# Performance work log

Measured on AMD Instinct MI355X. Metric: run time of the kernel, lower is better.

The kernel has to match this reference:

```python
import jax, jax.numpy as jnp
import numpy as np

NUM_HEADS = 32
NUM_KV_HEADS = 8
HEAD_DIM = 128
NEG_INF = -1e9


def rotate_half(x):
    x1, x2 = jnp.split(x, 2, axis=-1)
    return jnp.concatenate([-x2, x1], axis=-1)


def setup_inputs() -> dict:
    key = jax.random.key(0)
    ks = jax.random.split(key, 8)
    B, S, H = 2, 2048, 4096
    hidden_states = jax.random.normal(ks[0], (B, S, H), jnp.float32) * 0.02
    # additive causal mask [1,1,S,S]: 0 on/below diagonal, -1e9 above
    causal = jnp.tril(jnp.ones((S, S), bool))
    attention_mask = jnp.where(causal, 0.0, NEG_INF)[None, None, :, :].astype(jnp.float32)
    # RoPE tables (theta=500000 style), shape [1,S,head_dim]
    inv_freq = 1.0 / (500000.0 ** (np.arange(0, HEAD_DIM, 2, dtype=np.float32) / HEAD_DIM))
    t = np.arange(S, dtype=np.float32)
    freqs = np.outer(t, inv_freq)  # [S, head_dim/2]
    emb = np.concatenate([freqs, freqs], axis=-1)  # [S, head_dim]
    cos = jnp.asarray(np.cos(emb))[None]
    sin = jnp.asarray(np.sin(emb))[None]
    scale = 0.02
    wq = jax.random.normal(ks[1], (NUM_HEADS * HEAD_DIM, H), jnp.float32) * scale
    wk = jax.random.normal(ks[2], (NUM_KV_HEADS * HEAD_DIM, H), jnp.float32) * scale
    wv = jax.random.normal(ks[3], (NUM_KV_HEADS * HEAD_DIM, H), jnp.float32) * scale
    wo = jax.random.normal(ks[4], (H, NUM_HEADS * HEAD_DIM), jnp.float32) * scale
    return {"hidden_states": hidden_states, "attention_mask": attention_mask,
            "cos": cos, "sin": sin, "wq": wq, "wk": wk, "wv": wv, "wo": wo}


def reference(hidden_states, attention_mask, cos, sin, wq, wk, wv, wo):
    B, S, H = hidden_states.shape
    nh, nkv, hd = NUM_HEADS, NUM_KV_HEADS, HEAD_DIM
    groups = nh // nkv
    # QKV projections (bias=False)
    q = jnp.einsum('bsh,dh->bsd', hidden_states, wq).reshape(B, S, nh, hd).transpose(0, 2, 1, 3)
    k = jnp.einsum('bsh,dh->bsd', hidden_states, wk).reshape(B, S, nkv, hd).transpose(0, 2, 1, 3)
    v = jnp.einsum('bsh,dh->bsd', hidden_states, wv).reshape(B, S, nkv, hd).transpose(0, 2, 1, 3)
    # RoPE: cos/sin [1,S,hd] -> broadcast over head dim [1,1,S,hd]
    c = cos[:, None, :, :]
    s = sin[:, None, :, :]
    q = q * c + rotate_half(q) * s
    k = k * c + rotate_half(k) * s
    # GQA: repeat_kv
    k = jnp.repeat(k, groups, axis=1)  # [B,nh,S,hd]
    v = jnp.repeat(v, groups, axis=1)
    # SDPA with additive mask
    scores = jnp.einsum('bhqd,bhkd->bhqk', q, k) / jnp.sqrt(jnp.float32(hd))
    scores = scores + attention_mask[:, :, :, :k.shape[2]]
    attn = jax.nn.softmax(scores, axis=-1)
    out = jnp.einsum('bhqk,bhkd->bhqd', attn, v)  # [B,nh,S,hd]
    out = out.transpose(0, 2, 1, 3).reshape(B, S, nh * hd)
    return jnp.einsum('bsd,hd->bsh', out, wo)
```

## Files before the change

kernel.cpp:

```cpp
#include <hip/hip_runtime.h>
#include <hip/hip_bf16.h>

typedef __attribute__((ext_vector_type(8))) __bf16 bf16x8;
typedef __attribute__((ext_vector_type(4))) float f32x4;
typedef __attribute__((ext_vector_type(16))) float f32x16;
typedef __attribute__((ext_vector_type(4))) unsigned int u32x4;

#define SEQ 2048
#define NH 32
#define NKV 8
#define HD 128

__device__ __forceinline__ ushort f2bf(float f) {
  unsigned u = __builtin_bit_cast(unsigned, f);
  unsigned r = (u + 0x7fffu + ((u >> 16) & 1u)) >> 16;
  return (ushort)r;
}
__device__ __forceinline__ float bf2f(ushort h) {
  return __builtin_bit_cast(float, ((unsigned)h) << 16);
}
__device__ __forceinline__ unsigned cvt_pk_bf16(float lo, float hi) {
  unsigned r;
  asm("v_cvt_pk_bf16_f32 %0, %1, %2" : "=v"(r) : "v"(lo), "v"(hi));
  return r;
}
__device__ __forceinline__ float exp2_fast(float x) {
  float r;
  asm("v_exp_f32 %0, %1" : "=v"(r) : "v"(x));
  return r;
}
__device__ __forceinline__ void gload16(const void* g, void* l) {
  __builtin_amdgcn_global_load_lds(
      (const __attribute__((address_space(1))) void*)g,
      (__attribute__((address_space(3))) void*)l, 16, 0, 0);
}

__global__ __launch_bounds__(256) void f2bf5_kernel(const float4* __restrict__ hs,
                                                    const float4* __restrict__ wq,
                                                    const float4* __restrict__ wk,
                                                    const float4* __restrict__ wv,
                                                    const float4* __restrict__ wo,
                                                    ushort4* __restrict__ out) {
  unsigned i = blockIdx.x * 256 + threadIdx.x;
  const float4* src;
  unsigned j;
  if (i < 4194304u) { src = hs; j = i; }
  else if (i < 8388608u) { src = wq; j = i - 4194304u; }
  else if (i < 9437184u) { src = wk; j = i - 8388608u; }
  else if (i < 10485760u) { src = wv; j = i - 9437184u; }
  else { src = wo; j = i - 10485760u; }
  float4 v = src[j];
  ushort4 o;
  o.x = f2bf(v.x); o.y = f2bf(v.y); o.z = f2bf(v.z); o.w = f2bf(v.w);
  out[i] = o;
}

template <int OUTF32>
__global__ __launch_bounds__(256) void gemm_bt_kernel(const ushort* __restrict__ A,
                                                      const ushort* __restrict__ B,
                                                      void* __restrict__ C,
                                                      int M, int N, int K) {
  __shared__ ushort As[2][128 * 32];
  __shared__ ushort Bs[2][128 * 32];
  const int tid = threadIdx.x;
  const int w = tid >> 6, l = tid & 63;
  const int lr = l & 15, lc = l >> 4;
  const int bx = blockIdx.x, by = blockIdx.y;
  const int wr = w >> 1, wc = w & 1;

  f32x4 z = {0.f, 0.f, 0.f, 0.f};
  f32x4 acc[4][4];
#pragma unroll
  for (int i = 0; i < 4; ++i)
#pragma unroll
    for (int j = 0; j < 4; ++j) acc[i][j] = z;

  const ushort* aSrc = A + (size_t)(by * 128 + 32 * w + (l >> 2)) * K + (l & 3) * 8;
  const ushort* bSrc = B + (size_t)(bx * 128 + 32 * w + (l >> 2)) * K + (l & 3) * 8;
  const int ldsOff = (32 * w) * 32;

#pragma unroll
  for (int q = 0; q < 2; ++q) {
    gload16(aSrc + (size_t)q * 16 * K, &As[0][ldsOff + q * 512]);
    gload16(bSrc + (size_t)q * 16 * K, &Bs[0][ldsOff + q * 512]);
  }
  __syncthreads();

  const int nk = K >> 5;
  int cur = 0;
  for (int kt = 0; kt < nk; ++kt) {
    if (kt + 1 < nk) {
      const ushort* a2 = aSrc + (size_t)(kt + 1) * 32;
      const ushort* b2 = bSrc + (size_t)(kt + 1) * 32;
#pragma unroll
      for (int q = 0; q < 2; ++q) {
        gload16(a2 + (size_t)q * 16 * K, &As[cur ^ 1][ldsOff + q * 512]);
        gload16(b2 + (size_t)q * 16 * K, &Bs[cur ^ 1][ldsOff + q * 512]);
      }
    }
    bf16x8 af[4], bfr[4];
#pragma unroll
    for (int i = 0; i < 4; ++i)
      af[i] = *(const bf16x8*)&As[cur][(64 * wr + 16 * i + lr) * 32 + lc * 8];
#pragma unroll
    for (int j = 0; j < 4; ++j)
      bfr[j] = *(const bf16x8*)&Bs[cur][(64 * wc + 16 * j + lr) * 32 + lc * 8];
#pragma unroll
    for (int i = 0; i < 4; ++i)
#pragma unroll
      for (int j = 0; j < 4; ++j)
        acc[i][j] = __builtin_amdgcn_mfma_f32_16x16x32_bf16(af[i], bfr[j], acc[i][j], 0, 0, 0);
    __syncthreads();
    cur ^= 1;
  }

#pragma unroll
  for (int i = 0; i < 4; ++i)
#pragma unroll
    for (int j = 0; j < 4; ++j) {
      int row = by * 128 + 64 * wr + 16 * i + lc * 4;
      int col = bx * 128 + 64 * wc + 16 * j + lr;
#pragma unroll
      for (int r = 0; r < 4; ++r) {
        if (OUTF32)
          ((float*)C)[(size_t)(row + r) * N + col] = acc[i][j][r];
        else
          ((ushort*)C)[(size_t)(row + r) * N + col] = f2bf(acc[i][j][r]);
      }
    }
}

template <int OUTF32>
__global__ __launch_bounds__(512, 2) void gemm256_kernel(const ushort* __restrict__ A,
                                                         const ushort* __restrict__ B,
                                                         void* __restrict__ C,
                                                         int M, int N, int K) {
  __shared__ ushort As[2][256 * 64];
  __shared__ ushort Bs[2][256 * 64];
  const int tid = threadIdx.x;
  const int w = tid >> 6, l = tid & 63;
  const int lr = l & 15, lc = l >> 4;
  const int wr = w >> 2, wc = w & 3;

  const int nbx = N >> 8;
  const int cpx = gridDim.x >> 3;
  const int sw = (blockIdx.x & 7) * cpx + (blockIdx.x >> 3);
  const int bx = sw % nbx, by = sw / nbx;

  const ushort* Asrc = A + (size_t)(by * 256) * K;
  const ushort* Bsrc = B + (size_t)(bx * 256) * K;

  f32x4 z = {0.f, 0.f, 0.f, 0.f};
  f32x4 acc[8][4];
#pragma unroll
  for (int m = 0; m < 8; ++m)
#pragma unroll
    for (int n = 0; n < 4; ++n) acc[m][n] = z;

  const int NK = K >> 6;

  auto stage = [&](int kt2, int s) {
    if (kt2 >= NK) return;
    const int mat = s >> 1, half = s & 1;
    const ushort* g = mat ? Bsrc : Asrc;
    char* lb = (char*)(mat ? &Bs[kt2 & 1][0] : &As[kt2 & 1][0]) + half * 16384 + w * 1024;
#pragma unroll
    for (int i = 0; i < 2; ++i) {
      int row = half * 128 + i * 64 + w * 8 + (l >> 3);
      int csw = ((l & 7) * 16) ^ ((row & 7) << 4);
      gload16(g + (size_t)row * K + kt2 * 64 + (csw >> 1), lb + i * 8192);
    }
  };

  stage(0, 0); stage(0, 1); stage(0, 2); stage(0, 3);
  stage(1, 0);

  bf16x8 af[4][2], bfr[4][2];
  for (int kt = 0; kt < NK; ++kt) {
    const char* Ab = (const char*)&As[kt & 1][0];
    const char* Bb = (const char*)&Bs[kt & 1][0];
    if (kt + 1 < NK) asm volatile("s_waitcnt vmcnt(2)" ::: "memory");
    else             asm volatile("s_waitcnt vmcnt(0)" ::: "memory");
    asm volatile("s_barrier" ::: "memory");

#pragma unroll
    for (int m = 0; m < 4; ++m) {
      int row = wr * 128 + m * 16 + lr;
#pragma unroll
      for (int ks = 0; ks < 2; ++ks)
        af[m][ks] = *(const bf16x8*)(Ab + row * 128 + ((ks * 64 + lc * 16) ^ ((row & 7) << 4)));
    }
#pragma unroll
    for (int n = 0; n < 2; ++n) {
      int row = wc * 64 + n * 16 + lr;
#pragma unroll
      for (int ks = 0; ks < 2; ++ks)
        bfr[n][ks] = *(const bf16x8*)(Bb + row * 128 + ((ks * 64 + lc * 16) ^ ((row & 7) << 4)));
    }
    stage(kt + 1, 1);
    __builtin_amdgcn_s_setprio(1);
#pragma unroll
    for (int m = 0; m < 4; ++m)
#pragma unroll
      for (int n = 0; n < 2; ++n)
#pragma unroll
        for (int ks = 0; ks < 2; ++ks)
          acc[m][n] = __builtin_amdgcn_mfma_f32_16x16x32_bf16(af[m][ks], bfr[n][ks], acc[m][n], 0, 0, 0);
    __builtin_amdgcn_s_setprio(0);
    asm volatile("s_barrier" ::: "memory");

#pragma unroll
    for (int n = 2; n < 4; ++n) {
      int row = wc * 64 + n * 16 + lr;
#pragma unroll
      for (int ks = 0; ks < 2; ++ks)
        bfr[n][ks] = *(const bf16x8*)(Bb + row * 128 + ((ks * 64 + lc * 16) ^ ((row & 7) << 4)));
    }
    stage(kt + 1, 2);
    __builtin_amdgcn_s_setprio(1);
#pragma unroll
    for (int m = 0; m < 4; ++m)
#pragma unroll
      for (int n = 2; n < 4; ++n)
#pragma unroll
        for (int ks = 0; ks < 2; ++ks)
          acc[m][n] = __builtin_amdgcn_mfma_f32_16x16x32_bf16(af[m][ks], bfr[n][ks], acc[m][n], 0, 0, 0);
    __builtin_amdgcn_s_setprio(0);
    asm volatile("s_barrier" ::: "memory");

#pragma unroll
    for (int m = 0; m < 4; ++m) {
      int row = wr * 128 + (m + 4) * 16 + lr;
#pragma unroll
      for (int ks = 0; ks < 2; ++ks)
        af[m][ks] = *(const bf16x8*)(Ab + row * 128 + ((ks * 64 + lc * 16) ^ ((row & 7) << 4)));
    }
    stage(kt + 1, 3);
    __builtin_amdgcn_s_setprio(1);
#pragma unroll
    for (int m = 0; m < 4; ++m)
#pragma unroll
      for (int n = 0; n < 2; ++n)
#pragma unroll
        for (int ks = 0; ks < 2; ++ks)
          acc[m + 4][n] = __builtin_amdgcn_mfma_f32_16x16x32_bf16(af[m][ks], bfr[n][ks], acc[m + 4][n], 0, 0, 0);
    __builtin_amdgcn_s_setprio(0);
    asm volatile("s_barrier" ::: "memory");

    stage(kt + 2, 0);
    __builtin_amdgcn_s_setprio(1);
#pragma unroll
    for (int m = 0; m < 4; ++m)
#pragma unroll
      for (int n = 2; n < 4; ++n)
#pragma unroll
        for (int ks = 0; ks < 2; ++ks)
          acc[m + 4][n] = __builtin_amdgcn_mfma_f32_16x16x32_bf16(af[m][ks], bfr[n][ks], acc[m + 4][n], 0, 0, 0);
    __builtin_amdgcn_s_setprio(0);
  }

#pragma unroll
  for (int m = 0; m < 8; ++m)
#pragma unroll
    for (int n = 0; n < 4; ++n) {
      int row = by * 256 + wr * 128 + m * 16 + lc * 4;
      int col = bx * 256 + wc * 64 + n * 16 + lr;
#pragma unroll
      for (int r = 0; r < 4; ++r) {
        if (OUTF32)
          ((float*)C)[(size_t)(row + r) * N + col] = acc[m][n][r];
        else
          ((ushort*)C)[(size_t)(row + r) * N + col] = f2bf(acc[m][n][r]);
      }
    }
}

__global__ __launch_bounds__(256) void relayout_kernel(const ushort* __restrict__ q_lin,
                                                       const ushort* __restrict__ kv_lin,
                                                       const float* __restrict__ cosb,
                                                       const float* __restrict__ sinb,
                                                       ushort* __restrict__ Qh,
                                                       ushort* __restrict__ Kh,
                                                       ushort* __restrict__ Vt,
                                                       float qscale) {
  __shared__ ushort t[64][66];
  const unsigned bid = blockIdx.x;
  if (bid < 40960u) {
    const bool isQ = bid < 32768u;
    const ushort* in = isQ ? q_lin : kv_lin;
    ushort* out = isQ ? Qh : Kh;
    const int ld = isQ ? 4096 : 2048;
    const int hshift = isQ ? 5 : 3;
    const float scale = isQ ? qscale : 1.0f;
    int idx = (isQ ? bid : (bid - 32768u)) * 256 + threadIdx.x;
    int d = idx & 63;
    int nh = 1 << hshift;
    int h = (idx >> 6) & (nh - 1);
    int rowg = idx >> (6 + hshift);
    int s = rowg & (SEQ - 1);
    int b = rowg >> 11;
    const ushort* p = in + (size_t)rowg * ld + h * HD + d;
    float x = bf2f(p[0]), y = bf2f(p[64]);
    float c = cosb[s * HD + d], sn = sinb[s * HD + d];
    ushort* qo = out + (((size_t)(b * nh + h)) * SEQ + s) * HD + d;
    qo[0] = f2bf((x * c - y * sn) * scale);
    qo[64] = f2bf((y * c + x * sn) * scale);
  } else {
    unsigned i = bid - 40960u;
    const int s0 = (i & 31) * 64;
    const int c0 = ((i >> 5) & 15) * 64;
    const int b = i >> 9;
    const int tx = threadIdx.x & 63;
    const int ty = threadIdx.x >> 6;
#pragma unroll
    for (int rr = 0; rr < 64; rr += 4) {
      int r = rr + ty;
      t[r][tx] = kv_lin[((size_t)(b * SEQ + s0 + r)) * 2048 + 1024 + c0 + tx];
    }
    __syncthreads();
#pragma unroll
    for (int rr = 0; rr < 64; rr += 4) {
      int c = rr + ty;
      int cg = c0 + c;
      int kvh = cg >> 7, d = cg & 127;
      Vt[(((size_t)(b * NKV + kvh)) * HD + d) * SEQ + s0 + tx] = t[tx][c];
    }
  }
}

__global__ __launch_bounds__(512, 2) void attn_kernel(const ushort* __restrict__ Qh,
                                                      const ushort* __restrict__ Kh,
                                                      const ushort* __restrict__ Vt,
                                                      ushort* __restrict__ Out) {
  __shared__ ushort Kl[2][64 * 128];
  __shared__ ushort Vl[2][128 * 64];

  const int tid = threadIdx.x;
  const int w = tid >> 6, l = tid & 63;
  const int lq = l & 31;
  const int hl = l >> 5;
  const int g = w >> 2;
  const int wl = w & 3;

  const int n = blockIdx.x;
  const int xcd = n & 7, i = n >> 3;
  const int qpi = i & 7;
  const int h2 = (i >> 3) & 3;
  const int pp = 2 * xcd + (i >> 5);
  const int bb = pp >> 3, kvh = pp & 7;
  const int hh = kvh * 4 + h2;
  const int bh = bb * 32 + hh;
  const int qt = g ? (15 - qpi) : qpi;
  const int q0 = qt * 128;
  const int wrow0 = q0 + 32 * wl;
  const int qrow = wrow0 + lq;

  const ushort* Kbase = Kh + ((size_t)(bb * NKV + kvh) * SEQ) * HD;
  const ushort* Vbase = Vt + ((size_t)(bb * NKV + kvh) * HD) * SEQ;

  bf16x8 qf[8];
  {
    const ushort* qrp = Qh + ((size_t)bh * SEQ + qrow) * HD + 8 * hl;
#pragma unroll
    for (int s8 = 0; s8 < 8; ++s8) qf[s8] = *(const bf16x8*)(qrp + 16 * s8);
  }

  f32x16 o[4];
#pragma unroll
  for (int db = 0; db < 4; ++db)
#pragma unroll
    for (int i2 = 0; i2 < 16; ++i2) o[db][i2] = 0.f;
  float m_run = -1e30f, l_run = 0.f;

  const int ntw = 2 * qt + (wl >> 1) + 1;
  const int ntb = 2 * (15 - qpi) + 2;

  auto stageKV = [&](int buf, int t) {
    const int kv0 = t * 64;
#pragma unroll
    for (int q = 0; q < 2; ++q) {
      int c = 2 * w + q;
      int row = c * 4 + (l >> 4);
      int cs = ((l & 15) ^ (row & 7)) * 8;
      gload16(Kbase + ((size_t)(kv0 + row)) * HD + cs, &Kl[buf][c * 512]);
    }
#pragma unroll
    for (int q = 0; q < 2; ++q) {
      int c = 2 * w + q;
      int row = c * 8 + (l >> 3);
      int cs = ((l & 7) ^ (row & 7)) * 8;
      gload16(Vbase + (size_t)row * SEQ + kv0 + cs, &Vl[buf][c * 512]);
    }
  };

  stageKV(0, 0);
  __syncthreads();

  int cur = 0;
  for (int t = 0; t < ntb; ++t) {
    const int kv0 = t * 64;
    if (t + 1 < ntb) stageKV(cur ^ 1, t + 1);

    if (t < ntw) {
      f32x16 sacc[2];
#pragma unroll
      for (int b2 = 0; b2 < 2; ++b2)
#pragma unroll
        for (int i2 = 0; i2 < 16; ++i2) sacc[b2][i2] = 0.f;

      const int swz = lq & 7;
      __builtin_amdgcn_s_setprio(1);
#pragma unroll
      for (int s8 = 0; s8 < 8; ++s8) {
#pragma unroll
        for (int b2 = 0; b2 < 2; ++b2) {
          int row = 32 * b2 + lq;
          bf16x8 kf = *(const bf16x8*)((const char*)&Kl[cur][0] + row * 256 +
                                       (((2 * s8 + hl) ^ swz) << 4));
          sacc[b2] = __builtin_amdgcn_mfma_f32_32x32x16_bf16(kf, qf[s8], sacc[b2], 0, 0, 0);
        }
      }
      __builtin_amdgcn_s_setprio(0);

      if (t == ntw - 1) {
#pragma unroll
        for (int b2 = 0; b2 < 2; ++b2)
#pragma unroll
          for (int r2 = 0; r2 < 16; ++r2) {
            int kv = kv0 + 32 * b2 + (r2 & 3) + 8 * (r2 >> 2) + 4 * hl;
            if (kv > qrow) sacc[b2][r2] = -1e30f;
          }
      }

      float tm[8];
#pragma unroll
      for (int r2 = 0; r2 < 8; ++r2)
        tm[r2] = fmaxf(fmaxf(sacc[0][r2], sacc[0][r2 + 8]),
                       fmaxf(sacc[1][r2], sacc[1][r2 + 8]));
#pragma unroll
      for (int s2 = 4; s2; s2 >>= 1)
#pragma unroll
        for (int r2 = 0; r2 < s2; ++r2) tm[r2] = fmaxf(tm[r2], tm[r2 + s2]);
      float mx = fmaxf(tm[0], __shfl_xor(tm[0], 32));

      if (__any(mx > m_run + 8.0f)) {
        float mn = fmaxf(m_run, mx);
        float sc = exp2_fast(m_run - mn);
        m_run = mn;
        l_run *= sc;
#pragma unroll
        for (int db = 0; db < 4; ++db) o[db] *= sc;
      }

#pragma unroll
      for (int b2 = 0; b2 < 2; ++b2)
#pragma unroll
        for (int r2 = 0; r2 < 16; ++r2) sacc[b2][r2] = exp2_fast(sacc[b2][r2] - m_run);
      float ts[8];
#pragma unroll
      for (int r2 = 0; r2 < 8; ++r2)
        ts[r2] = (sacc[0][r2] + sacc[0][r2 + 8]) + (sacc[1][r2] + sacc[1][r2 + 8]);
#pragma unroll
      for (int s2 = 4; s2; s2 >>= 1)
#pragma unroll
        for (int r2 = 0; r2 < s2; ++r2) ts[r2] += ts[r2 + s2];
      l_run += ts[0] + __shfl_xor(ts[0], 32);

      unsigned pw[2][8];
#pragma unroll
      for (int b2 = 0; b2 < 2; ++b2)
#pragma unroll
        for (int i2 = 0; i2 < 8; ++i2)
          pw[b2][i2] = cvt_pk_bf16(sacc[b2][2 * i2], sacc[b2][2 * i2 + 1]);

#pragma unroll
      for (int s = 0; s < 4; ++s) {
        const int b2 = s >> 1, bs = 4 * (s & 1);
        unsigned wA = pw[b2][bs], wB = pw[b2][bs + 1], wC = pw[b2][bs + 2], wD = pw[b2][bs + 3];
        unsigned s1 = hl ? wA : wC, s2v = hl ? wB : wD;
        unsigned rx1 = (unsigned)__shfl_xor((int)s1, 32);
        unsigned rx2 = (unsigned)__shfl_xor((int)s2v, 32);
        u32x4 fw = {hl ? rx1 : wA, hl ? rx2 : wB, hl ? wC : rx1, hl ? wD : rx2};
        bf16x8 pfrag = __builtin_bit_cast(bf16x8, fw);
        bf16x8 vf[4];
#pragma unroll
        for (int db = 0; db < 4; ++db) {
          int row = 32 * db + lq;
          vf[db] = *(const bf16x8*)((const char*)&Vl[cur][0] + row * 128 +
                                    (((2 * s + hl) ^ swz) << 4));
        }
        __builtin_amdgcn_s_setprio(1);
#pragma unroll
        for (int db = 0; db < 4; ++db)
          o[db] = __builtin_amdgcn_mfma_f32_32x32x16_bf16(vf[db], pfrag, o[db], 0, 0, 0);
        __builtin_amdgcn_s_setprio(0);
      }
    }
    __syncthreads();
    cur ^= 1;
  }

  const float inv = 1.0f / l_run;
  ushort* outp = Out + ((size_t)bb * SEQ + qrow) * (NH * HD) + hh * HD;
#pragma unroll
  for (int db = 0; db < 4; ++db)
#pragma unroll
    for (int i2 = 0; i2 < 8; ++i2) {
      unsigned wrd = cvt_pk_bf16(o[db][2 * i2] * inv, o[db][2 * i2 + 1] * inv);
      int d = 32 * db + 2 * (i2 & 1) + 8 * (i2 >> 1) + 4 * hl;
      *(unsigned*)(outp + d) = wrd;
    }
}

extern "C" void kernel_launch(void* const* d_in, const int* in_sizes, int n_in,
                              void* d_out, int out_size, void* d_ws, size_t ws_size,
                              hipStream_t stream) {
  const float* hs = (const float*)d_in[0];
  const float* cosb = (const float*)d_in[2];
  const float* sinb = (const float*)d_in[3];
  const float* wq = (const float*)d_in[4];
  const float* wk = (const float*)d_in[5];
  const float* wv = (const float*)d_in[6];
  const float* wo = (const float*)d_in[7];

  char* ws = (char*)d_ws;
  ushort* hs_bf = (ushort*)(ws);
  ushort* wq_bf = (ushort*)(ws + 33554432);
  ushort* wk_bf = (ushort*)(ws + 67108864);
  ushort* wo_bf = (ushort*)(ws + 83886080);
  ushort* q_lin = (ushort*)(ws + 117440512);
  ushort* kv_lin = (ushort*)(ws + 150994944);
  ushort* Qh = hs_bf;
  ushort* Kh = wq_bf;
  ushort* Vt = (ushort*)(ws + 41943040);
  ushort* attn_out = q_lin;

  f2bf5_kernel<<<57344, 256, 0, stream>>>((const float4*)hs, (const float4*)wq,
                                          (const float4*)wk, (const float4*)wv,
                                          (const float4*)wo, (ushort4*)ws);

  gemm256_kernel<0><<<256, 512, 0, stream>>>(hs_bf, wq_bf, q_lin, 4096, 4096, 4096);
  gemm_bt_kernel<0><<<dim3(16, 32), 256, 0, stream>>>(hs_bf, wk_bf, kv_lin, 4096, 2048, 4096);

  relayout_kernel<<<41984, 256, 0, stream>>>(q_lin, kv_lin, cosb, sinb, Qh, Kh, Vt,
                                             0.08838834764831845f * 1.4426950408889634f);

  attn_kernel<<<512, 512, 0, stream>>>(Qh, Kh, Vt, attn_out);

  gemm256_kernel<1><<<256, 512, 0, stream>>>(attn_out, wo_bf, d_out, 4096, 4096, 4096);
}
```

Before: 525.0 us.

## Fuse Q RoPE into attention Q load and add barriers in GEMM stages

Removes the Q portion of the relayout kernel. The attention kernel now reads Q straight from the linear projection output and applies RoPE and the softmax scale in registers before building its MFMA fragments. This removes a full read and write pass over the Q tensor and shrinks the relayout launch. Separately, an s_barrier is added after each async staging call in the GEMM main loop, which adds synchronization and may reduce overlap. The attention output buffer is moved to avoid aliasing the still-needed q_lin buffer.

```diff
diff --git a/kernel.cpp b/kernel.cpp
--- a/kernel.cpp
+++ b/kernel.cpp
@@ -198,6 +198,7 @@
         bfr[n][ks] = *(const bf16x8*)(Bb + row * 128 + ((ks * 64 + lc * 16) ^ ((row & 7) << 4)));
     }
     stage(kt + 1, 1);
+    asm volatile("s_barrier" ::: "memory");
     __builtin_amdgcn_s_setprio(1);
 #pragma unroll
     for (int m = 0; m < 4; ++m)
@@ -217,6 +218,7 @@
         bfr[n][ks] = *(const bf16x8*)(Bb + row * 128 + ((ks * 64 + lc * 16) ^ ((row & 7) << 4)));
     }
     stage(kt + 1, 2);
+    asm volatile("s_barrier" ::: "memory");
     __builtin_amdgcn_s_setprio(1);
 #pragma unroll
     for (int m = 0; m < 4; ++m)
@@ -236,6 +238,7 @@
         af[m][ks] = *(const bf16x8*)(Ab + row * 128 + ((ks * 64 + lc * 16) ^ ((row & 7) << 4)));
     }
     stage(kt + 1, 3);
+    asm volatile("s_barrier" ::: "memory");
     __builtin_amdgcn_s_setprio(1);
 #pragma unroll
     for (int m = 0; m < 4; ++m)
@@ -248,6 +251,7 @@
     asm volatile("s_barrier" ::: "memory");
 
     stage(kt + 2, 0);
+    asm volatile("s_barrier" ::: "memory");
     __builtin_amdgcn_s_setprio(1);
 #pragma unroll
     for (int m = 0; m < 4; ++m)
@@ -275,38 +279,28 @@
     }
 }
 
-__global__ __launch_bounds__(256) void relayout_kernel(const ushort* __restrict__ q_lin,
-                                                       const ushort* __restrict__ kv_lin,
+__global__ __launch_bounds__(256) void relayout_kernel(const ushort* __restrict__ kv_lin,
                                                        const float* __restrict__ cosb,
                                                        const float* __restrict__ sinb,
-                                                       ushort* __restrict__ Qh,
                                                        ushort* __restrict__ Kh,
-                                                       ushort* __restrict__ Vt,
-                                                       float qscale) {
+                                                       ushort* __restrict__ Vt) {
   __shared__ ushort t[64][66];
   const unsigned bid = blockIdx.x;
-  if (bid < 40960u) {
-    const bool isQ = bid < 32768u;
-    const ushort* in = isQ ? q_lin : kv_lin;
-    ushort* out = isQ ? Qh : Kh;
-    const int ld = isQ ? 4096 : 2048;
-    const int hshift = isQ ? 5 : 3;
-    const float scale = isQ ? qscale : 1.0f;
-    int idx = (isQ ? bid : (bid - 32768u)) * 256 + threadIdx.x;
+  if (bid < 8192u) {
+    int idx = bid * 256 + threadIdx.x;
     int d = idx & 63;
-    int nh = 1 << hshift;
-    int h = (idx >> 6) & (nh - 1);
-    int rowg = idx >> (6 + hshift);
+    int h = (idx >> 6) & 7;
+    int rowg = idx >> 9;
     int s = rowg & (SEQ - 1);
     int b = rowg >> 11;
-    const ushort* p = in + (size_t)rowg * ld + h * HD + d;
+    const ushort* p = kv_lin + (size_t)rowg * 2048 + h * HD + d;
     float x = bf2f(p[0]), y = bf2f(p[64]);
     float c = cosb[s * HD + d], sn = sinb[s * HD + d];
-    ushort* qo = out + (((size_t)(b * nh + h)) * SEQ + s) * HD + d;
-    qo[0] = f2bf((x * c - y * sn) * scale);
-    qo[64] = f2bf((y * c + x * sn) * scale);
+    ushort* qo = Kh + (((size_t)(b * NKV + h)) * SEQ + s) * HD + d;
+    qo[0] = f2bf(x * c - y * sn);
+    qo[64] = f2bf(y * c + x * sn);
   } else {
-    unsigned i = bid - 40960u;
+    unsigned i = bid - 8192u;
     const int s0 = (i & 31) * 64;
     const int c0 = ((i >> 5) & 15) * 64;
     const int b = i >> 9;
@@ -328,10 +322,13 @@
   }
 }
 
-__global__ __launch_bounds__(512, 2) void attn_kernel(const ushort* __restrict__ Qh,
+__global__ __launch_bounds__(512, 2) void attn_kernel(const ushort* __restrict__ Qlin,
                                                       const ushort* __restrict__ Kh,
                                                       const ushort* __restrict__ Vt,
-                                                      ushort* __restrict__ Out) {
+                                                      const float* __restrict__ cosb,
+                                                      const float* __restrict__ sinb,
+                                                      ushort* __restrict__ Out,
+                                                      float qscale) {
   __shared__ ushort Kl[2][64 * 128];
   __shared__ ushort Vl[2][128 * 64];
 
@@ -349,7 +346,6 @@
   const int pp = 2 * xcd + (i >> 5);
   const int bb = pp >> 3, kvh = pp & 7;
   const int hh = kvh * 4 + h2;
-  const int bh = bb * 32 + hh;
   const int qt = g ? (15 - qpi) : qpi;
   const int q0 = qt * 128;
   const int wrow0 = q0 + 32 * wl;
@@ -360,9 +356,28 @@
 
   bf16x8 qf[8];
   {
-    const ushort* qrp = Qh + ((size_t)bh * SEQ + qrow) * HD + 8 * hl;
-#pragma unroll
-    for (int s8 = 0; s8 < 8; ++s8) qf[s8] = *(const bf16x8*)(qrp + 16 * s8);
+    const ushort* qrp = Qlin + ((size_t)(bb * SEQ) + qrow) * 4096 + hh * HD + 8 * hl;
+    const float* cb = cosb + qrow * HD + 8 * hl;
+    const float* sb = sinb + qrow * HD + 8 * hl;
+#pragma unroll
+    for (int p = 0; p < 4; ++p) {
+      u32x4 ua = __builtin_bit_cast(u32x4, *(const bf16x8*)(qrp + 16 * p));
+      u32x4 ub = __builtin_bit_cast(u32x4, *(const bf16x8*)(qrp + 16 * p + 64));
+      unsigned lo[4], hi[4];
+#pragma unroll
+      for (int jj = 0; jj < 4; ++jj) {
+        float x0 = bf2f((ushort)(ua[jj] & 0xffffu)), x1 = bf2f((ushort)(ua[jj] >> 16));
+        float y0 = bf2f((ushort)(ub[jj] & 0xffffu)), y1 = bf2f((ushort)(ub[jj] >> 16));
+        float cl0 = cb[16 * p + 2 * jj], cl1 = cb[16 * p + 2 * jj + 1];
+        float sl0 = sb[16 * p + 2 * jj], sl1 = sb[16 * p + 2 * jj + 1];
+        float ch0 = cb[16 * p + 64 + 2 * jj], ch1 = cb[16 * p + 64 + 2 * jj + 1];
+        float sh0 = sb[16 * p + 64 + 2 * jj], sh1 = sb[16 * p + 64 + 2 * jj + 1];
+        lo[jj] = cvt_pk_bf16((x0 * cl0 - y0 * sl0) * qscale, (x1 * cl1 - y1 * sl1) * qscale);
+        hi[jj] = cvt_pk_bf16((y0 * ch0 + x0 * sh0) * qscale, (y1 * ch1 + x1 * sh1) * qscale);
+      }
+      qf[p] = __builtin_bit_cast(bf16x8, (u32x4){lo[0], lo[1], lo[2], lo[3]});
+      qf[p + 4] = __builtin_bit_cast(bf16x8, (u32x4){hi[0], hi[1], hi[2], hi[3]});
+    }
   }
 
   f32x16 o[4];
@@ -530,10 +545,9 @@
   ushort* wo_bf = (ushort*)(ws + 83886080);
   ushort* q_lin = (ushort*)(ws + 117440512);
   ushort* kv_lin = (ushort*)(ws + 150994944);
-  ushort* Qh = hs_bf;
   ushort* Kh = wq_bf;
   ushort* Vt = (ushort*)(ws + 41943040);
-  ushort* attn_out = q_lin;
+  ushort* attn_out = hs_bf;
 
   f2bf5_kernel<<<57344, 256, 0, stream>>>((const float4*)hs, (const float4*)wq,
                                           (const float4*)wk, (const float4*)wv,
@@ -542,10 +556,10 @@
   gemm256_kernel<0><<<256, 512, 0, stream>>>(hs_bf, wq_bf, q_lin, 4096, 4096, 4096);
   gemm_bt_kernel<0><<<dim3(16, 32), 256, 0, stream>>>(hs_bf, wk_bf, kv_lin, 4096, 2048, 4096);
 
-  relayout_kernel<<<41984, 256, 0, stream>>>(q_lin, kv_lin, cosb, sinb, Qh, Kh, Vt,
-                                             0.08838834764831845f * 1.4426950408889634f);
-
-  attn_kernel<<<512, 512, 0, stream>>>(Qh, Kh, Vt, attn_out);
+  relayout_kernel<<<9216, 256, 0, stream>>>(kv_lin, cosb, sinb, Kh, Vt);
+
+  attn_kernel<<<512, 512, 0, stream>>>(q_lin, Kh, Vt, cosb, sinb, attn_out,
+                                       0.08838834764831845f * 1.4426950408889634f);
 
   gemm256_kernel<1><<<256, 512, 0, stream>>>(attn_out, wo_bf, d_out, 4096, 4096, 4096);
 }
```

Result: slower. 536.9 us (+2.3%).
